# Optimization experiments

Measured on AMD Instinct MI355X. Metric: run time of the kernel, lower is better.

Reference implementation:

```python
import jax, jax.numpy as jnp
from jax import lax
import numpy as np

B, CIN, COUT, S = 2, 64, 128, 12
H1, H2 = CIN * 4, COUT * 4          # MBConv hidden dims (expand_ratio=4)
HEADS = 8
MLP_HID = COUT * 4                   # transformer mlp_ratio=4
EPS = 1e-5


def conv1x1(x, w, b=None):
    # 1x1x1 Conv3d == channel matmul. w: [out, in], x: [B,C,H,W,D]
    y = jnp.einsum('oc,bchwd->bohwd', w, x)
    if b is not None:
        y = y + b[None, :, None, None, None]
    return y


def inorm(x, g, b):
    # InstanceNorm3d(affine=True): per-sample, per-channel over spatial dims
    m = x.mean(axis=(2, 3, 4), keepdims=True)
    v = x.var(axis=(2, 3, 4), keepdims=True)
    return (x - m) * jax.lax.rsqrt(v + EPS) * g[None, :, None, None, None] + b[None, :, None, None, None]


def gnorm(x, g, b, groups):
    Bb, C, H, W, D = x.shape
    xr = x.reshape(Bb, groups, C // groups, H, W, D)
    m = xr.mean(axis=(2, 3, 4, 5), keepdims=True)
    v = xr.var(axis=(2, 3, 4, 5), keepdims=True)
    xr = (xr - m) * jax.lax.rsqrt(v + EPS)
    return xr.reshape(Bb, C, H, W, D) * g[None, :, None, None, None] + b[None, :, None, None, None]


def dwconv3(x, w):
    # depthwise 3x3x3, stride 1, pad 1. w: [C,1,3,3,3]
    return lax.conv_general_dilated(
        x, w, window_strides=(1, 1, 1), padding=[(1, 1)] * 3,
        dimension_numbers=('NCDHW', 'OIDHW', 'NCDHW'),
        feature_group_count=x.shape[1])


def mbconv(x, ew, g1, b1, dw, g2, b2, sw1, sb1, sw2, sb2, pw, g3, b3, use_residual):
    res = x
    h = jax.nn.silu(inorm(conv1x1(x, ew), g1, b1))        # expand 1x1
    h = jax.nn.silu(inorm(dwconv3(h, dw), g2, b2))        # depthwise 3x3x3
    s = h.mean(axis=(2, 3, 4), keepdims=True)             # SE: squeeze
    s = jax.nn.silu(conv1x1(s, sw1, sb1))
    s = jax.nn.sigmoid(conv1x1(s, sw2, sb2))
    h = h * s
    h = inorm(conv1x1(h, pw), g3, b3)                     # project
    return res + h if use_residual else h


def mhsa(x, qkv_w, proj_w, proj_b):
    Bb, C, H, W, D = x.shape
    N = H * W * D
    hd = C // HEADS
    qkv = conv1x1(x, qkv_w).reshape(Bb, 3, HEADS, hd, N)
    qkv = jnp.transpose(qkv, (1, 0, 2, 4, 3))             # [3,B,h,N,hd]
    q, k, v = qkv[0], qkv[1], qkv[2]
    attn = jax.nn.softmax(jnp.einsum('bhnd,bhmd->bhnm', q, k) * (hd ** -0.5), axis=-1)
    out = jnp.einsum('bhnm,bhmd->bhnd', attn, v)          # [B,h,N,hd]
    out = jnp.transpose(out, (0, 1, 3, 2)).reshape(Bb, C, H, W, D)
    return conv1x1(out, proj_w, proj_b)


def transformer_block(x, n1g, n1b, qkv, pw, pb, n2g, n2b, mw1, mb1, mw2, mb2):
    x = x + mhsa(gnorm(x, n1g, n1b, min(32, x.shape[1])), qkv, pw, pb)
    h = gnorm(x, n2g, n2b, min(32, x.shape[1]))
    h = conv1x1(jax.nn.gelu(conv1x1(h, mw1, mb1), approximate=False), mw2, mb2)
    return x + h


def shuffle_attn(x, cw1, cw2, gng, gnb, sw):
    b, c, h, w, d = x.shape
    G = 4
    gc = c // (2 * G)  # group_channels
    x6 = x.reshape(b, G, 2 * gc, h, w, d)
    x0 = x6[:, :, :gc].reshape(b * G, gc, h, w, d)
    x1 = x6[:, :, gc:].reshape(b * G, gc, h, w, d)
    # channel branch
    a = x0.mean(axis=(2, 3, 4), keepdims=True)
    a = conv1x1(jax.nn.silu(conv1x1(a, cw1)), cw2)
    x0 = jax.nn.sigmoid(a) * x0
    # spatial branch: GroupNorm(max(1,gc//8)=2 groups) + 1x1 conv
    sgn = gnorm(x1, gng, gnb, max(1, gc // 8))
    x1 = jax.nn.sigmoid(conv1x1(sgn, sw)) * x1
    out = jnp.concatenate([x0.reshape(b, G * gc, h, w, d), x1.reshape(b, G * gc, h, w, d)], axis=1)
    # channel shuffle
    out = out.reshape(b, G, 2 * gc, h, w, d).transpose(0, 2, 1, 3, 4, 5).reshape(b, c, h, w, d)
    return out


def setup_inputs() -> dict:
    key = jax.random.key(0)
    ks = iter(jax.random.split(key, 64))
    w = lambda *shape: jax.random.normal(next(ks), shape, jnp.float32) * 0.05
    p = {}
    p['x'] = jax.random.normal(next(ks), (B, CIN, S, S, S), jnp.float32)
    # mbconv1 (in=64 -> hidden=256 -> out=128), SE reduced = 256//4 = 64
    r1 = H1 // 4
    p['m1_ew'] = w(H1, CIN); p['m1_g1'] = jnp.ones(H1); p['m1_b1'] = jnp.zeros(H1)
    p['m1_dw'] = w(H1, 1, 3, 3, 3); p['m1_g2'] = jnp.ones(H1); p['m1_b2'] = jnp.zeros(H1)
    p['m1_sw1'] = w(r1, H1); p['m1_sb1'] = jnp.zeros(r1)
    p['m1_sw2'] = w(H1, r1); p['m1_sb2'] = jnp.zeros(H1)
    p['m1_pw'] = w(COUT, H1); p['m1_g3'] = jnp.ones(COUT); p['m1_b3'] = jnp.zeros(COUT)
    # mbconv2 (in=128 -> hidden=512 -> out=128, residual), SE reduced = 512//4 = 128
    r2 = H2 // 4
    p['m2_ew'] = w(H2, COUT); p['m2_g1'] = jnp.ones(H2); p['m2_b1'] = jnp.zeros(H2)
    p['m2_dw'] = w(H2, 1, 3, 3, 3); p['m2_g2'] = jnp.ones(H2); p['m2_b2'] = jnp.zeros(H2)
    p['m2_sw1'] = w(r2, H2); p['m2_sb1'] = jnp.zeros(r2)
    p['m2_sw2'] = w(H2, r2); p['m2_sb2'] = jnp.zeros(H2)
    p['m2_pw'] = w(COUT, H2); p['m2_g3'] = jnp.ones(COUT); p['m2_b3'] = jnp.zeros(COUT)
    # transformer
    p['t_n1g'] = jnp.ones(COUT); p['t_n1b'] = jnp.zeros(COUT)
    p['t_qkv'] = w(3 * COUT, COUT)
    p['t_pw'] = w(COUT, COUT); p['t_pb'] = jnp.zeros(COUT)
    p['t_n2g'] = jnp.ones(COUT); p['t_n2b'] = jnp.zeros(COUT)
    p['t_mw1'] = w(MLP_HID, COUT); p['t_mb1'] = jnp.zeros(MLP_HID)
    p['t_mw2'] = w(COUT, MLP_HID); p['t_mb2'] = jnp.zeros(COUT)
    # shuffle attention: group_channels = 128 // 8 = 16, channel_fc reduces to 4
    gc = COUT // 8
    p['s_cw1'] = w(max(1, gc // 4), gc); p['s_cw2'] = w(gc, max(1, gc // 4))
    p['s_gng'] = jnp.ones(gc); p['s_gnb'] = jnp.zeros(gc)
    p['s_sw'] = w(gc, gc)
    return p


def reference(x, m1_ew, m1_g1, m1_b1, m1_dw, m1_g2, m1_b2, m1_sw1, m1_sb1, m1_sw2, m1_sb2, m1_pw, m1_g3, m1_b3, m2_ew, m2_g1, m2_b1, m2_dw, m2_g2, m2_b2, m2_sw1, m2_sb1, m2_sw2, m2_sb2, m2_pw, m2_g3, m2_b3, t_n1g, t_n1b, t_qkv, t_pw, t_pb, t_n2g, t_n2b, t_mw1, t_mb1, t_mw2, t_mb2, s_cw1, s_cw2, s_gng, s_gnb, s_sw):
    x = mbconv(x, m1_ew, m1_g1, m1_b1, m1_dw, m1_g2, m1_b2, m1_sw1, m1_sb1, m1_sw2, m1_sb2, m1_pw, m1_g3, m1_b3, use_residual=False)
    x = mbconv(x, m2_ew, m2_g1, m2_b1, m2_dw, m2_g2, m2_b2, m2_sw1, m2_sb1, m2_sw2, m2_sb2, m2_pw, m2_g3, m2_b3, use_residual=True)
    x = transformer_block(x, t_n1g, t_n1b, t_qkv, t_pw, t_pb, t_n2g, t_n2b, t_mw1, t_mb1, t_mw2, t_mb2)
    x = shuffle_attn(x, s_cw1, s_cw2, s_gng, s_gnb, s_sw)
    return x
```

## Files before the change

kernel.cpp:

```cpp
#include <hip/hip_runtime.h>
#include <cmath>

#define NSP 1728
#define BB  2
#define SS  12

typedef __attribute__((ext_vector_type(8))) short short8;
typedef __attribute__((ext_vector_type(4))) short short4v;
typedef __attribute__((ext_vector_type(4))) float floatx4;

__device__ __forceinline__ short f2bf(float f) {
    unsigned u = __float_as_uint(f);
    u += 0x7fff + ((u >> 16) & 1);
    return (short)(u >> 16);
}
__device__ __forceinline__ unsigned pack2bf(float a, float b) {
    unsigned ua = __float_as_uint(a); ua += 0x7fff + ((ua >> 16) & 1);
    unsigned ub = __float_as_uint(b); ub += 0x7fff + ((ub >> 16) & 1);
    return (ua >> 16) | (ub & 0xffff0000u);
}
__device__ __forceinline__ short8 ld8(const short* p) {
    short4v a = *(const short4v*)p;
    short4v b = *(const short4v*)(p + 4);
    return __builtin_shufflevector(a, b, 0, 1, 2, 3, 4, 5, 6, 7);
}
__device__ __forceinline__ float fexp2(float x) {
    float r;
    asm("v_exp_f32 %0, %1" : "=v"(r) : "v"(x));
    return r;
}

__device__ __forceinline__ void block_reduce2(float& s, float& s2) {
    __shared__ float red[8][2];
    __syncthreads();
    #pragma unroll
    for (int o = 32; o; o >>= 1) {
        s  += __shfl_down(s,  o, 64);
        s2 += __shfl_down(s2, o, 64);
    }
    int lane = threadIdx.x & 63, w = threadIdx.x >> 6;
    if (lane == 0) { red[w][0] = s; red[w][1] = s2; }
    __syncthreads();
    int nw = (blockDim.x + 63) >> 6;
    if (threadIdx.x == 0) {
        float a = 0.f, b = 0.f;
        for (int i = 0; i < nw; i++) { a += red[i][0]; b += red[i][1]; }
        red[0][0] = a; red[0][1] = b;
    }
    __syncthreads();
    s = red[0][0]; s2 = red[0][1];
}

#define WTOT 376832
__global__ __launch_bounds__(256) void prep_kernel(
        const float* __restrict__ s0, const float* __restrict__ s1,
        const float* __restrict__ s2, const float* __restrict__ s3,
        const float* __restrict__ s4, const float* __restrict__ s5,
        const float* __restrict__ s6, const float* __restrict__ s7,
        short* __restrict__ dst, float* __restrict__ stz,
        const float* __restrict__ w1a, const float* __restrict__ w2a,
        const float* __restrict__ w1b, const float* __restrict__ w2b,
        float* __restrict__ tsw) {
    if (blockIdx.x < 11) stz[blockIdx.x * 256 + threadIdx.x] = 0.f;
    if (blockIdx.x >= 368) {
        int e = (blockIdx.x - 368) * 1024 + threadIdx.x * 4;
        #pragma unroll
        for (int k = 0; k < 4; k++) {
            int idx = e + k;
            float v;
            if (idx < 16384) {
                int c = idx >> 6, r = idx & 63;
                v = w1a[r * 256 + c];
            } else if (idx < 32768) {
                int l = idx - 16384; int r = l >> 8, ci = l & 255;
                v = w2a[ci * 64 + r];
            } else if (idx < 98304) {
                int l = idx - 32768; int c = l >> 7, r = l & 127;
                v = w1b[r * 512 + c];
            } else {
                int l = idx - 98304; int r = l >> 9, ci = l & 511;
                v = w2b[ci * 128 + r];
            }
            tsw[idx] = v;
        }
        return;
    }
    const int offs[9] = {0, 16384, 49152, 114688, 180224, 229376, 245760, 311296, WTOT};
    const float* srcs[8] = {s0, s1, s2, s3, s4, s5, s6, s7};
    int e = blockIdx.x * 1024 + threadIdx.x * 4;
    #pragma unroll
    for (int k = 0; k < 4; k++) {
        int idx = e + k;
        int seg = 0;
        while (idx >= offs[seg + 1]) seg++;
        dst[idx] = f2bf(srcs[seg][idx - offs[seg]]);
    }
}

template<int CIN, int SER>
__global__ __launch_bounds__(1024) void segate_kernel(
        const float* __restrict__ pooled_in,
        const float* __restrict__ w1t, const float* __restrict__ b1,
        const float* __restrict__ w2t, const float* __restrict__ b2,
        float* __restrict__ gate) {
    __shared__ float pooled[CIN];
    __shared__ float hid[SER];
    __shared__ float part[1024];
    int b = blockIdx.x;
    int tid = threadIdx.x;
    if (tid < CIN) pooled[tid] = pooled_in[b * CIN + tid];
    __syncthreads();
    {
        constexpr int S = 1024 / SER;
        constexpr int CC = CIN / S;
        int r = tid % SER, s = tid / SER;
        const float* wp = w1t + (size_t)(s * CC) * SER + r;
        float a = 0.f;
        #pragma unroll 4
        for (int c = 0; c < CC; c++) a = fmaf(wp[(size_t)c * SER], pooled[s * CC + c], a);
        part[tid] = a;
    }
    __syncthreads();
    if (tid < SER) {
        constexpr int S = 1024 / SER;
        float h = b1[tid];
        #pragma unroll
        for (int s2 = 0; s2 < S; s2++) h += part[s2 * SER + tid];
        hid[tid] = h / (1.f + __expf(-h));
    }
    __syncthreads();
    {
        constexpr int T = 1024 / CIN;
        constexpr int RR = SER / T;
        int ci = tid % CIN, s = tid / CIN;
        const float* wp = w2t + (size_t)(s * RR) * CIN + ci;
        float a = 0.f;
        #pragma unroll 4
        for (int r = 0; r < RR; r++) a = fmaf(wp[(size_t)r * CIN], hid[s * RR + r], a);
        part[tid] = a;
    }
    __syncthreads();
    if (tid < CIN) {
        constexpr int T = 1024 / CIN;
        float g = b2[tid];
        #pragma unroll
        for (int s2 = 0; s2 < T; s2++) g += part[s2 * CIN + tid];
        gate[b * CIN + tid] = 1.f / (1.f + __expf(-g));
    }
}

template<int CIN, int COUT>
__global__ __launch_bounds__(256) void convm_kernel(
        const float* __restrict__ in, const short* __restrict__ wb,
        const float* __restrict__ biasc,
        const float* __restrict__ segate,
        const float* __restrict__ fstats, const float* __restrict__ fg,
        const float* __restrict__ fb, int fgs,
        const float* __restrict__ ing, const float* __restrict__ inb,
        const float* __restrict__ inres,
        const float* __restrict__ po, const float* __restrict__ pl,
        float* __restrict__ xout,
        const float* resid, float* out, float* stats_out,
        const float* __restrict__ statres, int act) {
    constexpr int XP = CIN + 8;
    __shared__ float sc[CIN];
    __shared__ float sh[CIN];
    __shared__ float sa[CIN];
    __shared__ float sbl[CIN];
    __shared__ float hid[128];
    __shared__ __align__(16) short xa[16 * XP];
    int flat = blockIdx.x;
    int b = flat / 108, mt = flat % 108;
    int n0 = mt * 16;
    int tid = threadIdx.x;

    if (po) {
        if (tid < 128) {
            int hh = tid >> 4, j = tid & 15;
            float l = 0.f;
            #pragma unroll
            for (int js = 0; js < 6; js++)
                l += pl[(size_t)((b * 8 + hh) * 6 + js) * NSP + n0 + j];
            hid[tid] = 1.f / l;
        }
        __syncthreads();
        #pragma unroll
        for (int i = 0; i < CIN / 64; i++) {
            int e = tid + i * 256;
            int ci = e >> 2;
            int jj = (e & 3) * 4;
            int hh = ci >> 4, d = ci & 15;
            float4 acc = {0.f, 0.f, 0.f, 0.f};
            #pragma unroll
            for (int js = 0; js < 6; js++) {
                float4 pv = *(const float4*)(po +
                    ((size_t)((b * 8 + hh) * 6 + js) * 16 + d) * NSP + n0 + jj);
                acc.x += pv.x; acc.y += pv.y; acc.z += pv.z; acc.w += pv.w;
            }
            float4 li = *(const float4*)(hid + hh * 16 + jj);
            xa[(jj + 0) * XP + ci] = f2bf(acc.x * li.x);
            xa[(jj + 1) * XP + ci] = f2bf(acc.y * li.y);
            xa[(jj + 2) * XP + ci] = f2bf(acc.z * li.z);
            xa[(jj + 3) * XP + ci] = f2bf(acc.w * li.w);
        }
        __syncthreads();
    } else {
    if (segate) {
        for (int c = tid; c < CIN; c += 256) {
            sc[c] = segate[b * CIN + c];
            sh[c] = 0.f;
        }
    } else if (ing) {
        for (int c = tid; c < CIN; c += 256) {
            const float* S = fstats + (size_t)(b * CIN + c) * 5;
            float A = S[0], Bq = S[1], Cq = S[2], Dq = S[3], Eq = S[4];
            const float N = (float)NSP;
            float mean = A / N, var = Bq / N - mean * mean;
            float a_ = ing[c] * rsqrtf(var + 1e-5f);
            float b_ = inb[c] - mean * a_;
            sa[c] = a_; sbl[c] = b_;
            sc[c] = a_ * A + b_ * N + Dq;
            sh[c] = a_ * a_ * Bq + 2.f * a_ * b_ * A + b_ * b_ * N
                  + 2.f * a_ * Cq + 2.f * b_ * Dq + Eq;
        }
        __syncthreads();
        float gS = 0.f, gS2 = 0.f;
        if (tid < CIN) {
            int g0 = (tid / fgs) * fgs;
            for (int k = 0; k < fgs; k++) { gS += sc[g0 + k]; gS2 += sh[g0 + k]; }
        }
        __syncthreads();
        if (tid < CIN) {
            float Ng = fgs * (float)NSP;
            float gm = gS / Ng, gv = gS2 / Ng - gm * gm;
            float s_ = rsqrtf(gv + 1e-5f) * fg[tid];
            sc[tid] = s_;
            sh[tid] = fb[tid] - gm * s_;
        }
    } else if (fstats) {
        for (int c = tid; c < CIN; c += 256) {
            int g0 = c / fgs;
            float S = 0.f, S2 = 0.f;
            for (int k = 0; k < fgs; k++) {
                S  += fstats[(b * CIN + g0 * fgs + k) * 2];
                S2 += fstats[(b * CIN + g0 * fgs + k) * 2 + 1];
            }
            float N = fgs * (float)NSP;
            float mean = S / N, var = S2 / N - mean * mean;
            float s = rsqrtf(var + 1e-5f) * fg[c];
            sc[c] = s;
            sh[c] = fb[c] - mean * s;
        }
    } else {
        for (int c = tid; c < CIN; c += 256) { sc[c] = 1.f; sh[c] = 0.f; }
    }
    __syncthreads();

    bool dosw = (xout != nullptr) && (blockIdx.y == 0);
    #pragma unroll
    for (int i = 0; i < CIN / 64; i++) {
        int e = tid + i * 256;
        int ci = e >> 2;
        int jj = (e & 3) * 4;
        size_t gi = ((size_t)b * CIN + ci) * NSP + n0 + jj;
        float4 v4 = *(const float4*)(in + gi);
        float v0, v1, v2, v3;
        if (ing) {
            float4 rr = *(const float4*)(inres + gi);
            float a_ = sa[ci], b_ = sbl[ci];
            float x0 = fmaf(v4.x, a_, b_) + rr.x;
            float x1 = fmaf(v4.y, a_, b_) + rr.y;
            float x2 = fmaf(v4.z, a_, b_) + rr.z;
            float x3 = fmaf(v4.w, a_, b_) + rr.w;
            if (dosw) {
                float4 o; o.x = x0; o.y = x1; o.z = x2; o.w = x3;
                *(float4*)(xout + gi) = o;
            }
            float s_ = sc[ci], h_ = sh[ci];
            v0 = fmaf(x0, s_, h_); v1 = fmaf(x1, s_, h_);
            v2 = fmaf(x2, s_, h_); v3 = fmaf(x3, s_, h_);
        } else {
            float s_ = sc[ci], h_ = sh[ci];
            v0 = fmaf(v4.x, s_, h_); v1 = fmaf(v4.y, s_, h_);
            v2 = fmaf(v4.z, s_, h_); v3 = fmaf(v4.w, s_, h_);
            if (dosw) {
                float4 o; o.x = v0; o.y = v1; o.z = v2; o.w = v3;
                *(float4*)(xout + gi) = o;
            }
        }
        xa[(jj + 0) * XP + ci] = f2bf(v0);
        xa[(jj + 1) * XP + ci] = f2bf(v1);
        xa[(jj + 2) * XP + ci] = f2bf(v2);
        xa[(jj + 3) * XP + ci] = f2bf(v3);
    }
    __syncthreads();
    }

    int lane = tid & 63, wv = tid >> 6;
    int col = lane & 15, quad = lane >> 4;
    short8 afr[CIN / 32];
    #pragma unroll
    for (int kc = 0; kc < CIN / 32; kc++)
        afr[kc] = ld8(xa + col * XP + kc * 32 + quad * 8);

    int cobase = blockIdx.y * 64 + wv * 16;
    int co = cobase + col;
    const short* wrow = wb + (size_t)co * CIN;
    floatx4 acc = {0.f, 0.f, 0.f, 0.f};
    #pragma unroll
    for (int kc = 0; kc < CIN / 32; kc++) {
        short8 bw = ld8(wrow + kc * 32 + quad * 8);
        acc = __builtin_amdgcn_mfma_f32_16x16x32_bf16(afr[kc], bw, acc, 0, 0, 0);
    }
    float bv = biasc ? biasc[co] : 0.f;
    float r0 = acc[0] + bv, r1 = acc[1] + bv, r2 = acc[2] + bv, r3 = acc[3] + bv;
    if (act == 2) {
        r0 = 0.5f * r0 * (1.f + erff(r0 * 0.70710678118654752f));
        r1 = 0.5f * r1 * (1.f + erff(r1 * 0.70710678118654752f));
        r2 = 0.5f * r2 * (1.f + erff(r2 * 0.70710678118654752f));
        r3 = 0.5f * r3 * (1.f + erff(r3 * 0.70710678118654752f));
    }
    size_t oi = ((size_t)b * COUT + co) * NSP + n0 + quad * 4;
    if (resid) {
        float4 rv = *(const float4*)(resid + oi);
        r0 += rv.x; r1 += rv.y; r2 += rv.z; r3 += rv.w;
    }
    float4 ov; ov.x = r0; ov.y = r1; ov.z = r2; ov.w = r3;
    *(float4*)(out + oi) = ov;
    if (stats_out) {
        if (statres) {
            float4 rv = *(const float4*)(statres + oi);
            float s   = (r0 + r1) + (r2 + r3);
            float s2  = (r0 * r0 + r1 * r1) + (r2 * r2 + r3 * r3);
            float sx  = (r0 * rv.x + r1 * rv.y) + (r2 * rv.z + r3 * rv.w);
            float sr  = (rv.x + rv.y) + (rv.z + rv.w);
            float sr2 = (rv.x * rv.x + rv.y * rv.y) + (rv.z * rv.z + rv.w * rv.w);
            s   += __shfl_xor(s,   16, 64); s   += __shfl_xor(s,   32, 64);
            s2  += __shfl_xor(s2,  16, 64); s2  += __shfl_xor(s2,  32, 64);
            sx  += __shfl_xor(sx,  16, 64); sx  += __shfl_xor(sx,  32, 64);
            sr  += __shfl_xor(sr,  16, 64); sr  += __shfl_xor(sr,  32, 64);
            sr2 += __shfl_xor(sr2, 16, 64); sr2 += __shfl_xor(sr2, 32, 64);
            if (lane < 16) {
                float* sp = stats_out + (size_t)(b * COUT + cobase + lane) * 5;
                atomicAdd(sp + 0, s);
                atomicAdd(sp + 1, s2);
                atomicAdd(sp + 2, sx);
                atomicAdd(sp + 3, sr);
                atomicAdd(sp + 4, sr2);
            }
        } else {
            float s  = (r0 + r1) + (r2 + r3);
            float s2 = (r0 * r0 + r1 * r1) + (r2 * r2 + r3 * r3);
            s  += __shfl_xor(s,  16, 64);
            s  += __shfl_xor(s,  32, 64);
            s2 += __shfl_xor(s2, 16, 64);
            s2 += __shfl_xor(s2, 32, 64);
            if (lane < 16) {
                atomicAdd(&stats_out[(b * COUT + cobase + lane) * 2],     s);
                atomicAdd(&stats_out[(b * COUT + cobase + lane) * 2 + 1], s2);
            }
        }
    }
}

__global__ __launch_bounds__(256) void indw_kernel(
        const float* __restrict__ in,
        const float* __restrict__ g1, const float* __restrict__ b1,
        const float* __restrict__ dw,
        const float* __restrict__ g2, const float* __restrict__ b2,
        float* __restrict__ out, float* __restrict__ se_s, int C) {
    int bc = blockIdx.x;
    int c  = bc % C;
    __shared__ float tile[14 * 14 * 14];
    __shared__ float wsh[27];
    const float* ip = in + (size_t)bc * NSP;
    float r[7];
    float s = 0.f, s2 = 0.f;
    for (int i = threadIdx.x; i < 2744; i += 256) tile[i] = 0.f;
    #pragma unroll
    for (int i = 0; i < 7; i++) {
        int n = threadIdx.x + i * 256;
        if (n < NSP) { r[i] = ip[n]; s += r[i]; s2 += r[i] * r[i]; }
        else r[i] = 0.f;
    }
    if (threadIdx.x < 27) wsh[threadIdx.x] = dw[(size_t)c * 27 + threadIdx.x];
    block_reduce2(s, s2);
    float mean = s / NSP, var = s2 / NSP - (s / NSP) * (s / NSP);
    float rstd = rsqrtf(var + 1e-5f);
    float gc = g1[c], bc1 = b1[c];
    #pragma unroll
    for (int i = 0; i < 7; i++) {
        int n = threadIdx.x + i * 256;
        if (n < NSP) {
            int z = n / 144, y = (n / 12) % 12, x = n % 12;
            float v = (r[i] - mean) * rstd * gc + bc1;
            tile[((z + 1) * 14 + y + 1) * 14 + x + 1] = v / (1.f + __expf(-v));
        }
    }
    __syncthreads();
    float d[7];
    #pragma unroll
    for (int i = 0; i < 7; i++) {
        int n = threadIdx.x + i * 256;
        d[i] = 0.f;
        if (n < NSP) {
            int z = n / 144, y = (n / 12) % 12, x = n % 12;
            const float* ctr = tile + ((z + 1) * 14 + y + 1) * 14 + x + 1;
            float acc = 0.f;
            #pragma unroll
            for (int dz = 0; dz < 3; dz++)
                #pragma unroll
                for (int dy = 0; dy < 3; dy++)
                    #pragma unroll
                    for (int dx = 0; dx < 3; dx++)
                        acc = fmaf(wsh[dz * 9 + dy * 3 + dx],
                                   ctr[(dz - 1) * 196 + (dy - 1) * 14 + (dx - 1)], acc);
            d[i] = acc;
        }
    }
    s = 0.f; s2 = 0.f;
    #pragma unroll
    for (int i = 0; i < 7; i++) {
        int n = threadIdx.x + i * 256;
        if (n < NSP) { s += d[i]; s2 += d[i] * d[i]; }
    }
    block_reduce2(s, s2);
    mean = s / NSP; var = s2 / NSP - mean * mean;
    rstd = rsqrtf(var + 1e-5f);
    float gc2 = g2[c], bc2 = b2[c];
    float ssum = 0.f;
    float* op = out + (size_t)bc * NSP;
    #pragma unroll
    for (int i = 0; i < 7; i++) {
        int n = threadIdx.x + i * 256;
        if (n < NSP) {
            float v = (d[i] - mean) * rstd * gc2 + bc2;
            v = v / (1.f + __expf(-v));
            op[n] = v;
            ssum += v;
        }
    }
    float dummy = 0.f;
    block_reduce2(ssum, dummy);
    if (threadIdx.x == 0) se_s[bc] = ssum / NSP;
}

#define AKT 20
#define AVT 296
#define APT 36
#define JCH 288
__global__ __launch_bounds__(256) void attn_split_kernel(const float* __restrict__ qkv,
                                                         float* __restrict__ po,
                                                         float* __restrict__ pl) {
    __shared__ __align__(16) short kt[JCH * AKT];
    __shared__ __align__(16) short vt[16 * AVT];
    __shared__ __align__(16) short pt[4][16 * APT];
    int bh = blockIdx.x;
    int b = bh >> 3, h = bh & 7;
    int js = blockIdx.z;
    int j0 = js * JCH;
    const float* base = qkv + (size_t)b * 384 * NSP;
    const float* qp = base + (size_t)(h * 16) * NSP;
    const float* kp = base + (size_t)(128 + h * 16) * NSP;
    const float* vp = base + (size_t)(256 + h * 16) * NSP;
    for (int t = threadIdx.x; t < 16 * 144; t += 256) {
        int d = t / 144, j = (t - d * 144) * 2;
        float2 kv2 = *(const float2*)(kp + (size_t)d * NSP + j0 + j);
        float2 vv2 = *(const float2*)(vp + (size_t)d * NSP + j0 + j);
        kt[j * AKT + d]       = f2bf(kv2.x);
        kt[(j + 1) * AKT + d] = f2bf(kv2.y);
        *(unsigned*)(vt + d * AVT + j) = pack2bf(vv2.x, vv2.y);
    }
    int wave = threadIdx.x >> 6, lane = threadIdx.x & 63;
    int m = lane & 15, quad = lane >> 4;
    int q0 = (blockIdx.y * 4 + wave) * 16;
    short* ptw = pt[wave];
    short8 qa;
    #pragma unroll
    for (int i = 0; i < 8; i++) qa[i] = 0;
    if (quad < 2) {
        #pragma unroll
        for (int i = 0; i < 8; i++) {
            int d = quad * 8 + i;
            qa[i] = f2bf(qp[(size_t)d * NSP + q0 + m] * 0.36067376022224085f);
        }
    }
    __syncthreads();
    floatx4 o = {0.f, 0.f, 0.f, 0.f};
    float ls = 0.f;
    for (int s = 0; s < 9; s++) {
        int jl = s * 32;
        short8 ak0, ak1;
        #pragma unroll
        for (int i = 0; i < 8; i++) { ak0[i] = 0; ak1[i] = 0; }
        if (quad < 2) {
            ak0 = ld8(kt + (jl + m) * AKT + quad * 8);
            ak1 = ld8(kt + (jl + 16 + m) * AKT + quad * 8);
        }
        floatx4 s0 = {0.f, 0.f, 0.f, 0.f}, s1 = {0.f, 0.f, 0.f, 0.f};
        s0 = __builtin_amdgcn_mfma_f32_16x16x32_bf16(ak0, qa, s0, 0, 0, 0);
        s1 = __builtin_amdgcn_mfma_f32_16x16x32_bf16(ak1, qa, s1, 0, 0, 0);
        float p0r0 = fexp2(s0[0]), p0r1 = fexp2(s0[1]), p0r2 = fexp2(s0[2]), p0r3 = fexp2(s0[3]);
        float p1r0 = fexp2(s1[0]), p1r1 = fexp2(s1[1]), p1r2 = fexp2(s1[2]), p1r3 = fexp2(s1[3]);
        ls += (p0r0 + p0r1) + (p0r2 + p0r3) + (p1r0 + p1r1) + (p1r2 + p1r3);
        uint2 w0, w1;
        w0.x = pack2bf(p0r0, p0r1); w0.y = pack2bf(p0r2, p0r3);
        w1.x = pack2bf(p1r0, p1r1); w1.y = pack2bf(p1r2, p1r3);
        *(uint2*)(ptw + m * APT + quad * 4)      = w0;
        *(uint2*)(ptw + m * APT + 16 + quad * 4) = w1;
        short8 av = ld8(vt + m * AVT + jl + quad * 8);
        short8 pb = ld8(ptw + m * APT + quad * 8);
        o = __builtin_amdgcn_mfma_f32_16x16x32_bf16(av, pb, o, 0, 0, 0);
    }
    ls += __shfl_xor(ls, 16, 64);
    ls += __shfl_xor(ls, 32, 64);
    size_t pbase = ((size_t)(bh * 6 + js) * 16) * NSP;
    #pragma unroll
    for (int r = 0; r < 4; r++)
        po[pbase + (size_t)(quad * 4 + r) * NSP + q0 + m] = o[r];
    if (quad == 0) pl[(size_t)(bh * 6 + js) * NSP + q0 + m] = ls;
}

__global__ void sfinal_kernel(const float* __restrict__ X,
                              const float* __restrict__ st,
                              const float* __restrict__ cw1,
                              const float* __restrict__ cw2,
                              const float* __restrict__ gng,
                              const float* __restrict__ gnb,
                              const float* __restrict__ sw,
                              float* __restrict__ out) {
    int bg = blockIdx.x;
    int b = bg >> 2, g = bg & 3;
    __shared__ float swl[256];
    for (int i = threadIdx.x; i < 256; i += 64) swl[i] = sw[i];
    __syncthreads();
    float pooled[16];
    #pragma unroll
    for (int j = 0; j < 16; j++)
        pooled[j] = st[(b * 128 + g * 32 + j) * 2] * (1.f / NSP);
    float hid[4];
    #pragma unroll
    for (int r = 0; r < 4; r++) {
        float a = 0.f;
        #pragma unroll
        for (int j = 0; j < 16; j++) a = fmaf(cw1[r * 16 + j], pooled[j], a);
        hid[r] = a / (1.f + __expf(-a));
    }
    float gate[16];
    #pragma unroll
    for (int j = 0; j < 16; j++) {
        float a = 0.f;
        #pragma unroll
        for (int r = 0; r < 4; r++) a = fmaf(cw2[j * 4 + r], hid[r], a);
        gate[j] = 1.f / (1.f + __expf(-a));
    }
    float gmean[2], grstd[2];
    #pragma unroll
    for (int t = 0; t < 2; t++) {
        float S = 0.f, S2 = 0.f;
        #pragma unroll
        for (int k = 0; k < 8; k++) {
            int c = g * 32 + 16 + t * 8 + k;
            S  += st[(b * 128 + c) * 2];
            S2 += st[(b * 128 + c) * 2 + 1];
        }
        float N = 8.f * NSP;
        gmean[t] = S / N;
        grstd[t] = rsqrtf(S2 / N - gmean[t] * gmean[t] + 1e-5f);
    }
    int n = blockIdx.y * 64 + threadIdx.x;
    const float* xb = X + (size_t)b * 128 * NSP;
    #pragma unroll
    for (int j = 0; j < 16; j++) {
        float v = xb[(size_t)(g * 32 + j) * NSP + n] * gate[j];
        int k = g * 16 + j;
        int cp = (k % 32) * 4 + (k / 32);
        out[((size_t)b * 128 + cp) * NSP + n] = v;
    }
    float sgn[16];
    #pragma unroll
    for (int j = 0; j < 16; j++) {
        int grp = j >> 3;
        float xv = xb[(size_t)(g * 32 + 16 + j) * NSP + n];
        sgn[j] = (xv - gmean[grp]) * grstd[grp] * gng[j] + gnb[j];
    }
    #pragma unroll
    for (int j = 0; j < 16; j++) {
        float a = 0.f;
        #pragma unroll
        for (int jp = 0; jp < 16; jp++) a = fmaf(swl[j * 16 + jp], sgn[jp], a);
        float v = (1.f / (1.f + __expf(-a))) * xb[(size_t)(g * 32 + 16 + j) * NSP + n];
        int k = 64 + g * 16 + j;
        int cp = (k % 32) * 4 + (k / 32);
        out[((size_t)b * 128 + cp) * NSP + n] = v;
    }
}

extern "C" void kernel_launch(void* const* d_in, const int* in_sizes, int n_in,
                              void* d_out, int out_size, void* d_ws, size_t ws_size,
                              hipStream_t stream) {
    const float* x     = (const float*)d_in[0];
    const float* m1_ew = (const float*)d_in[1];
    const float* m1_g1 = (const float*)d_in[2];
    const float* m1_b1 = (const float*)d_in[3];
    const float* m1_dw = (const float*)d_in[4];
    const float* m1_g2 = (const float*)d_in[5];
    const float* m1_b2 = (const float*)d_in[6];
    const float* m1_sw1= (const float*)d_in[7];
    const float* m1_sb1= (const float*)d_in[8];
    const float* m1_sw2= (const float*)d_in[9];
    const float* m1_sb2= (const float*)d_in[10];
    const float* m1_pw = (const float*)d_in[11];
    const float* m1_g3 = (const float*)d_in[12];
    const float* m1_b3 = (const float*)d_in[13];
    const float* m2_ew = (const float*)d_in[14];
    const float* m2_g1 = (const float*)d_in[15];
    const float* m2_b1 = (const float*)d_in[16];
    const float* m2_dw = (const float*)d_in[17];
    const float* m2_g2 = (const float*)d_in[18];
    const float* m2_b2 = (const float*)d_in[19];
    const float* m2_sw1= (const float*)d_in[20];
    const float* m2_sb1= (const float*)d_in[21];
    const float* m2_sw2= (const float*)d_in[22];
    const float* m2_sb2= (const float*)d_in[23];
    const float* m2_pw = (const float*)d_in[24];
    const float* m2_g3 = (const float*)d_in[25];
    const float* m2_b3 = (const float*)d_in[26];
    const float* t_n1g = (const float*)d_in[27];
    const float* t_n1b = (const float*)d_in[28];
    const float* t_qkv = (const float*)d_in[29];
    const float* t_pw  = (const float*)d_in[30];
    const float* t_pb  = (const float*)d_in[31];
    const float* t_n2g = (const float*)d_in[32];
    const float* t_n2b = (const float*)d_in[33];
    const float* t_mw1 = (const float*)d_in[34];
    const float* t_mb1 = (const float*)d_in[35];
    const float* t_mw2 = (const float*)d_in[36];
    const float* t_mb2 = (const float*)d_in[37];
    const float* s_cw1 = (const float*)d_in[38];
    const float* s_cw2 = (const float*)d_in[39];
    const float* s_gng = (const float*)d_in[40];
    const float* s_gnb = (const float*)d_in[41];
    const float* s_sw  = (const float*)d_in[42];

    float* out = (float*)d_out;

    float* ws = (float*)d_ws;
    float* bufA   = ws;
    float* bufB   = bufA + (size_t)BB * 512 * NSP;
    float* bufX   = bufB + (size_t)BB * 512 * NSP;
    float* bufY   = bufX + (size_t)BB * 128 * NSP;
    float* bufQKV = bufY + (size_t)BB * 128 * NSP;
    float* pl     = bufQKV + (size_t)BB * 384 * NSP;
    float* small  = pl + (size_t)16 * 6 * NSP;
    float* se_s   = small;
    float* st1    = small + 1024;
    float* st3    = small + 1536;
    float* st4    = small + 2048;
    float* st2    = small + 2560;
    float* gate1  = small + 4096;
    float* gate2  = small + 4608;
    short* wbf    = (short*)(small + 8192);
    float* tsw    = small + 196608;
    float* T_M1SW1 = tsw;
    float* T_M1SW2 = tsw + 16384;
    float* T_M2SW1 = tsw + 32768;
    float* T_M2SW2 = tsw + 98304;
    float* bufX2  = tsw + 163840;
    float* po     = bufA;

    short* W_M1EW = wbf + 0;
    short* W_M1PW = wbf + 16384;
    short* W_M2EW = wbf + 49152;
    short* W_M2PW = wbf + 114688;
    short* W_QKV  = wbf + 180224;
    short* W_TPW  = wbf + 229376;
    short* W_MW1  = wbf + 245760;
    short* W_MW2  = wbf + 311296;

    dim3 blk(256);

    prep_kernel<<<528, blk, 0, stream>>>(
        m1_ew, m1_pw, m2_ew, m2_pw, t_qkv, t_pw, t_mw1, t_mw2, wbf, st1,
        m1_sw1, m1_sw2, m2_sw1, m2_sw2, tsw);

    convm_kernel<64, 256><<<dim3(BB * 108, 4), blk, 0, stream>>>(
        x, W_M1EW, nullptr,
        nullptr,
        nullptr, nullptr, nullptr, 0,
        nullptr, nullptr, nullptr,
        nullptr, nullptr, nullptr,
        nullptr, bufA, nullptr, nullptr, 0);
    indw_kernel<<<BB * 256, blk, 0, stream>>>(bufA, m1_g1, m1_b1, m1_dw, m1_g2, m1_b2, bufB, se_s, 256);
    segate_kernel<256, 64><<<BB, dim3(1024), 0, stream>>>(
        se_s, T_M1SW1, m1_sb1, T_M1SW2, m1_sb2, gate1);
    convm_kernel<256, 128><<<dim3(BB * 108, 2), blk, 0, stream>>>(
        bufB, W_M1PW, nullptr,
        gate1,
        nullptr, nullptr, nullptr, 0,
        nullptr, nullptr, nullptr,
        nullptr, nullptr, nullptr,
        nullptr, bufY, st1, nullptr, 0);

    convm_kernel<128, 512><<<dim3(BB * 108, 8), blk, 0, stream>>>(
        bufY, W_M2EW, nullptr,
        nullptr,
        st1, m1_g3, m1_b3, 1,
        nullptr, nullptr, nullptr,
        nullptr, nullptr, bufX,
        nullptr, bufA, nullptr, nullptr, 0);
    indw_kernel<<<BB * 512, blk, 0, stream>>>(bufA, m2_g1, m2_b1, m2_dw, m2_g2, m2_b2, bufB, se_s, 512);
    segate_kernel<512, 128><<<BB, dim3(1024), 0, stream>>>(
        se_s, T_M2SW1, m2_sb1, T_M2SW2, m2_sb2, gate2);
    convm_kernel<512, 128><<<dim3(BB * 108, 2), blk, 0, stream>>>(
        bufB, W_M2PW, nullptr,
        gate2,
        nullptr, nullptr, nullptr, 0,
        nullptr, nullptr, nullptr,
        nullptr, nullptr, nullptr,
        nullptr, bufY, st2, bufX, 0);

    convm_kernel<128, 384><<<dim3(BB * 108, 6), blk, 0, stream>>>(
        bufY, W_QKV, nullptr,
        nullptr,
        st2, t_n1g, t_n1b, 4,
        m2_g3, m2_b3, bufX,
        nullptr, nullptr, bufX2,
        nullptr, bufQKV, nullptr, nullptr, 0);
    attn_split_kernel<<<dim3(16, 27, 6), blk, 0, stream>>>(bufQKV, po, pl);
    convm_kernel<128, 128><<<dim3(BB * 108, 2), blk, 0, stream>>>(
        nullptr, W_TPW, t_pb,
        nullptr,
        nullptr, nullptr, nullptr, 0,
        nullptr, nullptr, nullptr,
        po, pl, nullptr,
        bufX2, bufX2, st3, nullptr, 0);
    convm_kernel<128, 512><<<dim3(BB * 108, 8), blk, 0, stream>>>(
        bufX2, W_MW1, t_mb1,
        nullptr,
        st3, t_n2g, t_n2b, 4,
        nullptr, nullptr, nullptr,
        nullptr, nullptr, nullptr,
        nullptr, bufA, nullptr, nullptr, 2);
    convm_kernel<512, 128><<<dim3(BB * 108, 2), blk, 0, stream>>>(
        bufA, W_MW2, t_mb2,
        nullptr,
        nullptr, nullptr, nullptr, 0,
        nullptr, nullptr, nullptr,
        nullptr, nullptr, nullptr,
        bufX2, bufX2, st4, nullptr, 0);

    sfinal_kernel<<<dim3(BB * 4, 27), dim3(64), 0, stream>>>(
        bufX2, st4, s_cw1, s_cw2, s_gng, s_gnb, s_sw, out);
}
```

Measured before the change: 316.7 us.

## Emit bf16 attention-ready QKV and MLP hidden layouts directly from conv epilogues

```diff
diff --git a/kernel.cpp b/kernel.cpp
--- a/kernel.cpp
+++ b/kernel.cpp
@@ -151,7 +151,8 @@
 
 template<int CIN, int COUT>
 __global__ __launch_bounds__(256) void convm_kernel(
-        const float* __restrict__ in, const short* __restrict__ wb,
+        const float* __restrict__ in, const short* __restrict__ inbf,
+        const short* __restrict__ wb,
         const float* __restrict__ biasc,
         const float* __restrict__ segate,
         const float* __restrict__ fstats, const float* __restrict__ fg,
@@ -160,8 +161,9 @@
         const float* __restrict__ inres,
         const float* __restrict__ po, const float* __restrict__ pl,
         float* __restrict__ xout,
-        const float* resid, float* out, float* stats_out,
-        const float* __restrict__ statres, int act) {
+        const float* resid, float* out,
+        short* __restrict__ obf, int obfm,
+        float* stats_out, const float* __restrict__ statres, int act) {
     constexpr int XP = CIN + 8;
     __shared__ float sc[CIN];
     __shared__ float sh[CIN];
@@ -174,6 +176,7 @@
     int n0 = mt * 16;
     int tid = threadIdx.x;
 
+    if (!inbf) {
     if (po) {
         if (tid < 128) {
             int hh = tid >> 4, j = tid & 15;
@@ -295,13 +298,21 @@
     }
     __syncthreads();
     }
+    }
 
     int lane = tid & 63, wv = tid >> 6;
     int col = lane & 15, quad = lane >> 4;
     short8 afr[CIN / 32];
-    #pragma unroll
-    for (int kc = 0; kc < CIN / 32; kc++)
-        afr[kc] = ld8(xa + col * XP + kc * 32 + quad * 8);
+    if (inbf) {
+        const short* ar = inbf + ((size_t)b * 1728 + n0 + col) * CIN;
+        #pragma unroll
+        for (int kc = 0; kc < CIN / 32; kc++)
+            afr[kc] = ld8(ar + kc * 32 + quad * 8);
+    } else {
+        #pragma unroll
+        for (int kc = 0; kc < CIN / 32; kc++)
+            afr[kc] = ld8(xa + col * XP + kc * 32 + quad * 8);
+    }
 
     int cobase = blockIdx.y * 64 + wv * 16;
     int co = cobase + col;
@@ -325,8 +336,35 @@
         float4 rv = *(const float4*)(resid + oi);
         r0 += rv.x; r1 += rv.y; r2 += rv.z; r3 += rv.w;
     }
-    float4 ov; ov.x = r0; ov.y = r1; ov.z = r2; ov.w = r3;
-    *(float4*)(out + oi) = ov;
+    if (obf) {
+        if (obfm == 1) {
+            if (co < 256) {
+                float s_ = (co < 128) ? 0.36067376022224085f : 1.f;
+                short* qb = obf + (((size_t)(b * 16 + (co >> 4)) * 1728 + n0 + quad * 4) * 16
+                                   + (co & 15));
+                qb[0]  = f2bf(r0 * s_);
+                qb[16] = f2bf(r1 * s_);
+                qb[32] = f2bf(r2 * s_);
+                qb[48] = f2bf(r3 * s_);
+            } else {
+                short* vb = obf + 884736
+                    + ((size_t)(b * 8 + ((co - 256) >> 4)) * 16 + (co & 15)) * 1728
+                    + n0 + quad * 4;
+                uint2 pv; pv.x = pack2bf(r0, r1); pv.y = pack2bf(r2, r3);
+                *(uint2*)vb = pv;
+            }
+        } else {
+            short* hb = obf + ((size_t)b * 1728 + n0 + quad * 4) * COUT + co;
+            hb[0]        = f2bf(r0);
+            hb[COUT]     = f2bf(r1);
+            hb[2 * COUT] = f2bf(r2);
+            hb[3 * COUT] = f2bf(r3);
+        }
+    }
+    if (out) {
+        float4 ov; ov.x = r0; ov.y = r1; ov.z = r2; ov.w = r3;
+        *(float4*)(out + oi) = ov;
+    }
     if (stats_out) {
         if (statres) {
             float4 rv = *(const float4*)(statres + oi);
@@ -445,57 +483,38 @@
     if (threadIdx.x == 0) se_s[bc] = ssum / NSP;
 }
 
-#define AKT 20
-#define AVT 296
 #define APT 36
 #define JCH 288
-__global__ __launch_bounds__(256) void attn_split_kernel(const float* __restrict__ qkv,
-                                                         float* __restrict__ po,
-                                                         float* __restrict__ pl) {
-    __shared__ __align__(16) short kt[JCH * AKT];
-    __shared__ __align__(16) short vt[16 * AVT];
+__global__ __launch_bounds__(256) void attn_split_kernel(
+        const short* __restrict__ qkbf, const short* __restrict__ vbf,
+        float* __restrict__ po, float* __restrict__ pl) {
     __shared__ __align__(16) short pt[4][16 * APT];
     int bh = blockIdx.x;
     int b = bh >> 3, h = bh & 7;
     int js = blockIdx.z;
     int j0 = js * JCH;
-    const float* base = qkv + (size_t)b * 384 * NSP;
-    const float* qp = base + (size_t)(h * 16) * NSP;
-    const float* kp = base + (size_t)(128 + h * 16) * NSP;
-    const float* vp = base + (size_t)(256 + h * 16) * NSP;
-    for (int t = threadIdx.x; t < 16 * 144; t += 256) {
-        int d = t / 144, j = (t - d * 144) * 2;
-        float2 kv2 = *(const float2*)(kp + (size_t)d * NSP + j0 + j);
-        float2 vv2 = *(const float2*)(vp + (size_t)d * NSP + j0 + j);
-        kt[j * AKT + d]       = f2bf(kv2.x);
-        kt[(j + 1) * AKT + d] = f2bf(kv2.y);
-        *(unsigned*)(vt + d * AVT + j) = pack2bf(vv2.x, vv2.y);
-    }
     int wave = threadIdx.x >> 6, lane = threadIdx.x & 63;
     int m = lane & 15, quad = lane >> 4;
     int q0 = (blockIdx.y * 4 + wave) * 16;
     short* ptw = pt[wave];
+    const short* qrow  = qkbf + ((size_t)(b * 16 + h) * 1728 + q0 + m) * 16;
+    const short* kbase = qkbf + ((size_t)(b * 16 + 8 + h) * 1728 + j0) * 16;
+    const short* vbase = vbf + ((size_t)(b * 8 + h) * 16) * 1728 + j0;
     short8 qa;
     #pragma unroll
     for (int i = 0; i < 8; i++) qa[i] = 0;
-    if (quad < 2) {
-        #pragma unroll
-        for (int i = 0; i < 8; i++) {
-            int d = quad * 8 + i;
-            qa[i] = f2bf(qp[(size_t)d * NSP + q0 + m] * 0.36067376022224085f);
-        }
-    }
-    __syncthreads();
+    if (quad < 2) qa = ld8(qrow + quad * 8);
     floatx4 o = {0.f, 0.f, 0.f, 0.f};
     float ls = 0.f;
+    #pragma unroll
     for (int s = 0; s < 9; s++) {
         int jl = s * 32;
         short8 ak0, ak1;
         #pragma unroll
         for (int i = 0; i < 8; i++) { ak0[i] = 0; ak1[i] = 0; }
         if (quad < 2) {
-            ak0 = ld8(kt + (jl + m) * AKT + quad * 8);
-            ak1 = ld8(kt + (jl + 16 + m) * AKT + quad * 8);
+            ak0 = ld8(kbase + (jl + m) * 16 + quad * 8);
+            ak1 = ld8(kbase + (jl + 16 + m) * 16 + quad * 8);
         }
         floatx4 s0 = {0.f, 0.f, 0.f, 0.f}, s1 = {0.f, 0.f, 0.f, 0.f};
         s0 = __builtin_amdgcn_mfma_f32_16x16x32_bf16(ak0, qa, s0, 0, 0, 0);
@@ -508,7 +527,7 @@
         w1.x = pack2bf(p1r0, p1r1); w1.y = pack2bf(p1r2, p1r3);
         *(uint2*)(ptw + m * APT + quad * 4)      = w0;
         *(uint2*)(ptw + m * APT + 16 + quad * 4) = w1;
-        short8 av = ld8(vt + m * AVT + jl + quad * 8);
+        short8 av = ld8(vbase + (size_t)m * 1728 + jl + quad * 8);
         short8 pb = ld8(ptw + m * APT + quad * 8);
         o = __builtin_amdgcn_mfma_f32_16x16x32_bf16(av, pb, o, 0, 0, 0);
     }
@@ -668,6 +687,8 @@
     float* T_M2SW2 = tsw + 98304;
     float* bufX2  = tsw + 163840;
     float* po     = bufA;
+    short* qkbf   = (short*)bufQKV;
+    short* hbf    = (short*)bufA;
 
     short* W_M1EW = wbf + 0;
     short* W_M1PW = wbf + 16384;
@@ -685,70 +706,62 @@
         m1_sw1, m1_sw2, m2_sw1, m2_sw2, tsw);
 
     convm_kernel<64, 256><<<dim3(BB * 108, 4), blk, 0, stream>>>(
-        x, W_M1EW, nullptr,
-        nullptr,
+        x, nullptr, W_M1EW, nullptr, nullptr,
         nullptr, nullptr, nullptr, 0,
         nullptr, nullptr, nullptr,
         nullptr, nullptr, nullptr,
-        nullptr, bufA, nullptr, nullptr, 0);
+        nullptr, bufA, nullptr, 0, nullptr, nullptr, 0);
     indw_kernel<<<BB * 256, blk, 0, stream>>>(bufA, m1_g1, m1_b1, m1_dw, m1_g2, m1_b2, bufB, se_s, 256);
     segate_kernel<256, 64><<<BB, dim3(1024), 0, stream>>>(
         se_s, T_M1SW1, m1_sb1, T_M1SW2, m1_sb2, gate1);
     convm_kernel<256, 128><<<dim3(BB * 108, 2), blk, 0, stream>>>(
-        bufB, W_M1PW, nullptr,
-        gate1,
+        bufB, nullptr, W_M1PW, nullptr, gate1,
         nullptr, nullptr, nullptr, 0,
         nullptr, nullptr, nullptr,
         nullptr, nullptr, nullptr,
-        nullptr, bufY, st1, nullptr, 0);
+        nullptr, bufY, nullptr, 0, st1, nullptr, 0);
 
     convm_kernel<128, 512><<<dim3(BB * 108, 8), blk, 0, stream>>>(
-        bufY, W_M2EW, nullptr,
-        nullptr,
+        bufY, nullptr, W_M2EW, nullptr, nullptr,
         st1, m1_g3, m1_b3, 1,
         nullptr, nullptr, nullptr,
         nullptr, nullptr, bufX,
-        nullptr, bufA, nullptr, nullptr, 0);
+        nullptr, bufA, nullptr, 0, nullptr, nullptr, 0);
     indw_kernel<<<BB * 512, blk, 0, stream>>>(bufA, m2_g1, m2_b1, m2_dw, m2_g2, m2_b2, bufB, se_s, 512);
     segate_kernel<512, 128><<<BB, dim3(1024), 0, stream>>>(
         se_s, T_M2SW1, m2_sb1, T_M2SW2, m2_sb2, gate2);
     convm_kernel<512, 128><<<dim3(BB * 108, 2), blk, 0, stream>>>(
-        bufB, W_M2PW, nullptr,
-        gate2,
+        bufB, nullptr, W_M2PW, nullptr, gate2,
         nullptr, nullptr, nullptr, 0,
         nullptr, nullptr, nullptr,
         nullptr, nullptr, nullptr,
-        nullptr, bufY, st2, bufX, 0);
+        nullptr, bufY, nullptr, 0, st2, bufX, 0);
 
     convm_kernel<128, 384><<<dim3(BB * 108, 6), blk, 0, stream>>>(
-        bufY, W_QKV, nullptr,
-        nullptr,
+        bufY, nullptr, W_QKV, nullptr, nullptr,
         st2, t_n1g, t_n1b, 4,
         m2_g3, m2_b3, bufX,
         nullptr, nullptr, bufX2,
-        nullptr, bufQKV, nullptr, nullptr, 0);
-    attn_split_kernel<<<dim3(16, 27, 6), blk, 0, stream>>>(bufQKV, po, pl);
+        nullptr, nullptr, qkbf, 1, nullptr, nullptr, 0);
+    attn_split_kernel<<<dim3(16, 27, 6), blk, 0, stream>>>(qkbf, qkbf + 884736, po, pl);
     convm_kernel<128, 128><<<dim3(BB * 108, 2), blk, 0, stream>>>(
-        nullptr, W_TPW, t_pb,
-        nullptr,
+        nullptr, nullptr, W_TPW, t_pb, nullptr,
         nullptr, nullptr, nullptr, 0,
         nullptr, nullptr, nullptr,
         po, pl, nullptr,
-        bufX2, bufX2, st3, nullptr, 0);
+        bufX2, bufX2, nullptr, 0, st3, nullptr, 0);
     convm_kernel<128, 512><<<dim3(BB * 108, 8), blk, 0, stream>>>(
-        bufX2, W_MW1, t_mb1,
-        nullptr,
+        bufX2, nullptr, W_MW1, t_mb1, nullptr,
         st3, t_n2g, t_n2b, 4,
         nullptr, nullptr, nullptr,
         nullptr, nullptr, nullptr,
-        nullptr, bufA, nullptr, nullptr, 2);
+        nullptr, nullptr, hbf, 2, nullptr, nullptr, 2);
     convm_kernel<512, 128><<<dim3(BB * 108, 2), blk, 0, stream>>>(
-        bufA, W_MW2, t_mb2,
-        nullptr,
+        nullptr, hbf, W_MW2, t_mb2, nullptr,
         nullptr, nullptr, nullptr, 0,
         nullptr, nullptr, nullptr,
         nullptr, nullptr, nullptr,
-        bufX2, bufX2, st4, nullptr, 0);
+        bufX2, bufX2, nullptr, 0, st4, nullptr, 0);
 
     sfinal_kernel<<<dim3(BB * 4, 27), dim3(64), 0, stream>>>(
         bufX2, st4, s_cw1, s_cw2, s_gng, s_gnb, s_sw, out);
```

Result: no change. 316.0 us (median of 2 runs) (-0.2%).
